# Kernel tuning notes

Hardware: AMD Instinct MI355X
Metric: run time of the kernel (lower is better)

Reference implementation:

```python
import jax, jax.numpy as jnp
import numpy as np

LN_EPS = 1e-5

def setup_inputs() -> dict:
    key = jax.random.key(0)
    ks = jax.random.split(key, 8)
    B, N, C = 8, 16384, 256
    x = jax.random.normal(ks[0], (B, N, C), dtype=jnp.float32)
    time_decay = jax.random.normal(ks[1], (C,), dtype=jnp.float32) * 0.1
    s = 1.0 / np.sqrt(C)
    W_k = jax.random.normal(ks[2], (C, C), dtype=jnp.float32) * s
    W_v = jax.random.normal(ks[3], (C, C), dtype=jnp.float32) * s
    W_r = jax.random.normal(ks[4], (C, C), dtype=jnp.float32) * s
    W_o = jax.random.normal(ks[5], (C, C), dtype=jnp.float32) * s
    ln_w = jnp.ones((C,), dtype=jnp.float32)
    ln_b = jnp.zeros((C,), dtype=jnp.float32)
    return {"x": x, "time_decay": time_decay, "W_k": W_k, "W_v": W_v,
            "W_r": W_r, "W_o": W_o, "ln_w": ln_w, "ln_b": ln_b}

def _layernorm(x, w, b):
    mu = jnp.mean(x, axis=-1, keepdims=True)
    var = jnp.mean(jnp.square(x - mu), axis=-1, keepdims=True)
    return (x - mu) * jax.lax.rsqrt(var + LN_EPS) * w + b

def reference(x, time_decay, W_k, W_v, W_r, W_o, ln_w, ln_b):
    # x: (B, N, C)
    xn = _layernorm(x, ln_w, ln_b)
    k = jnp.einsum('bnc,dc->bnd', xn, W_k)
    v = jnp.einsum('bnc,dc->bnd', xn, W_v)
    r = jax.nn.sigmoid(jnp.einsum('bnc,dc->bnd', xn, W_r))
    decay = jnp.exp(-jax.nn.relu(time_decay))  # (C,)

    def step(state, k_t):
        state = state * decay + k_t  # (B, C)
        return state, state

    k_tm = jnp.swapaxes(k, 0, 1)  # (N, B, C) time-major for scan
    init = jnp.zeros(k.shape[::2], dtype=x.dtype)  # (B, C)
    _, states = jax.lax.scan(step, init, k_tm)
    states = jnp.swapaxes(states, 0, 1)  # (B, N, C)
    y = r * (states + v)
    y = jnp.einsum('bnc,dc->bnd', y, W_o)
    return y
```

## Files before the change

### kernel.cpp

```cpp
#include <hip/hip_runtime.h>
#include <hip/hip_bf16.h>
#include <stdint.h>


typedef __attribute__((ext_vector_type(8))) short short8;
typedef __attribute__((ext_vector_type(4))) float f32x4;

static __device__ __forceinline__ unsigned short f2bf(float f) {
  __hip_bfloat16 h = __float2bfloat16(f);
  return *reinterpret_cast<unsigned short*>(&h);
}
static __device__ __forceinline__ float bf2f(unsigned short u) {
  unsigned int v = ((unsigned int)u) << 16;
  float f;
  __builtin_memcpy(&f, &v, 4);
  return f;
}

__global__ void ln_kernel(const float* __restrict__ x,
                          const float* __restrict__ w,
                          const float* __restrict__ b,
                          unsigned short* __restrict__ xn) {
  const int wv = threadIdx.x >> 6;
  const int ln = threadIdx.x & 63;
  const size_t row = (size_t)blockIdx.x * 4 + wv;
  const float4 v = reinterpret_cast<const float4*>(x)[row * 64 + ln];
  float s  = v.x + v.y + v.z + v.w;
  float sq = v.x * v.x + v.y * v.y + v.z * v.z + v.w * v.w;
#pragma unroll
  for (int off = 32; off; off >>= 1) {
    s  += __shfl_xor(s, off, 64);
    sq += __shfl_xor(sq, off, 64);
  }
  const float mu  = s * (1.0f / 256.0f);
  const float var = sq * (1.0f / 256.0f) - mu * mu;
  const float rs  = rsqrtf(var + 1e-5f);
  const float4 w4 = reinterpret_cast<const float4*>(w)[ln];
  const float4 b4 = reinterpret_cast<const float4*>(b)[ln];
  ushort4 o;
  o.x = f2bf((v.x - mu) * rs * w4.x + b4.x);
  o.y = f2bf((v.y - mu) * rs * w4.y + b4.y);
  o.z = f2bf((v.z - mu) * rs * w4.z + b4.z);
  o.w = f2bf((v.w - mu) * rs * w4.w + b4.w);
  reinterpret_cast<ushort4*>(xn)[row * 64 + ln] = o;
}

__global__ void cvt_weights(const float* __restrict__ Wk,
                            const float* __restrict__ Wv,
                            const float* __restrict__ Wr,
                            const float* __restrict__ Wo,
                            unsigned short* __restrict__ Wkvr,
                            unsigned short* __restrict__ Wob) {
  const int idx = blockIdx.x * 256 + threadIdx.x;
  if (idx < 768 * 256) {
    const int r = idx >> 8;
    const int c = idx & 255;
    const float* src = (r < 256) ? Wk : ((r < 512) ? Wv : Wr);
    Wkvr[idx] = f2bf(src[(r & 255) * 256 + c]);
  } else {
    const int j = idx - 768 * 256;
    Wob[j] = f2bf(Wo[j]);
  }
}

template <int EPI, int NY>
__global__ __launch_bounds__(512, 4) void gemm_bt(
    const unsigned short* __restrict__ A,
    const unsigned short* __restrict__ Bt,
    unsigned short* __restrict__ kbuf,
    unsigned short* __restrict__ vbuf,
    unsigned short* __restrict__ rbuf,
    float* __restrict__ outf) {
  constexpr int K = 256;
  __shared__ unsigned short Als[128][64];
  __shared__ unsigned short Bls[256][64];

  const int tid = threadIdx.x;
  const int wv = tid >> 6;
  const int ln = tid & 63;
  const int cpx = (int)gridDim.x >> 3;
  const int hw = (int)blockIdx.x;
  const int bid = (hw & 7) * cpx + (hw >> 3);
  const int bm0 = (bid / NY) * 128;
  const int bn0 = (bid % NY) * 256;
  const int lq = ln >> 4;
  const int lm = ln & 15;

  f32x4 acc[4][4];
#pragma unroll
  for (int i = 0; i < 4; ++i)
#pragma unroll
    for (int j = 0; j < 4; ++j) acc[i][j] = (f32x4){0.f, 0.f, 0.f, 0.f};

  const int m0w = (wv >> 2) * 64;
  const int n0w = (wv & 3) * 64;

  const int srow = ln >> 3;
  const int schunk = (ln & 7) ^ srow;

  const int ra = wv * 16;
  const int rb = wv * 32;

  for (int kk0 = 0; kk0 < K; kk0 += 64) {
    {
      const unsigned short* gA =
          A + (size_t)(bm0 + ra + srow) * K + kk0 + schunk * 8;
      __builtin_amdgcn_global_load_lds(
          (const __attribute__((address_space(1))) void*)gA,
          (__attribute__((address_space(3))) void*)&Als[ra][0], 16, 0, 0);
      __builtin_amdgcn_global_load_lds(
          (const __attribute__((address_space(1))) void*)(gA + 8 * K),
          (__attribute__((address_space(3))) void*)&Als[ra + 8][0], 16, 0, 0);
      const unsigned short* gB =
          Bt + (size_t)(bn0 + rb + srow) * K + kk0 + schunk * 8;
      __builtin_amdgcn_global_load_lds(
          (const __attribute__((address_space(1))) void*)gB,
          (__attribute__((address_space(3))) void*)&Bls[rb][0], 16, 0, 0);
      __builtin_amdgcn_global_load_lds(
          (const __attribute__((address_space(1))) void*)(gB + 8 * K),
          (__attribute__((address_space(3))) void*)&Bls[rb + 8][0], 16, 0, 0);
      __builtin_amdgcn_global_load_lds(
          (const __attribute__((address_space(1))) void*)(gB + 16 * K),
          (__attribute__((address_space(3))) void*)&Bls[rb + 16][0], 16, 0, 0);
      __builtin_amdgcn_global_load_lds(
          (const __attribute__((address_space(1))) void*)(gB + 24 * K),
          (__attribute__((address_space(3))) void*)&Bls[rb + 24][0], 16, 0, 0);
    }
    __syncthreads();
#pragma unroll
    for (int kk = 0; kk < 64; kk += 32) {
      short8 af[4], bfr[4];
      const int chunk = (kk >> 3) + lq;
      const int sw = chunk ^ (lm & 7);
#pragma unroll
      for (int t = 0; t < 4; ++t) {
        af[t] = *reinterpret_cast<const short8*>(&Als[m0w + t * 16 + lm][sw * 8]);
        bfr[t] = *reinterpret_cast<const short8*>(&Bls[n0w + t * 16 + lm][sw * 8]);
      }
#pragma unroll
      for (int mt = 0; mt < 4; ++mt)
#pragma unroll
        for (int nt = 0; nt < 4; ++nt)
          acc[mt][nt] = __builtin_amdgcn_mfma_f32_16x16x32_bf16(
              bfr[nt], af[mt], acc[mt][nt], 0, 0, 0);
    }
    __syncthreads();
  }

#pragma unroll
  for (int mt = 0; mt < 4; ++mt) {
    const int m_g = bm0 + m0w + mt * 16 + lm;
#pragma unroll
    for (int nt = 0; nt < 4; ++nt) {
      const int col = n0w + nt * 16 + lq * 4;
      f32x4 a = acc[mt][nt];
      if (EPI == 0) {
        const int bufi = bn0 >> 8;
        unsigned short* dst = (bufi == 0) ? kbuf : ((bufi == 1) ? vbuf : rbuf);
        if (bufi == 2) {
#pragma unroll
          for (int r = 0; r < 4; ++r) a[r] = 1.0f / (1.0f + __expf(-a[r]));
        }
        ushort4 pk;
        pk.x = f2bf(a[0]); pk.y = f2bf(a[1]); pk.z = f2bf(a[2]); pk.w = f2bf(a[3]);
        *reinterpret_cast<ushort4*>(&dst[(size_t)m_g * 256 + col]) = pk;
      } else {
        float4 o = make_float4(a[0], a[1], a[2], a[3]);
        *reinterpret_cast<float4*>(&outf[(size_t)m_g * 256 + col]) = o;
      }
    }
  }
}

__global__ void scan_carry(const unsigned short* __restrict__ k,
                           const float* __restrict__ td,
                           float* __restrict__ carry) {
  const int lane32 = threadIdx.x & 31;
  const int sub = threadIdx.x >> 5;
  const int bch = blockIdx.x * 8 + sub;
  const int c0 = lane32 * 8;
  float d[8], s[8];
#pragma unroll
  for (int j = 0; j < 8; ++j) {
    d[j] = expf(-fmaxf(td[c0 + j], 0.0f));
    s[j] = 0.0f;
  }
  const unsigned short* kp = k + (size_t)bch * 64 * 256 + c0;
#pragma unroll 4
  for (int i = 0; i < 64; ++i) {
    short8 kv = *reinterpret_cast<const short8*>(kp + (size_t)i * 256);
#pragma unroll
    for (int j = 0; j < 8; ++j) s[j] = s[j] * d[j] + bf2f((unsigned short)kv[j]);
  }
  float4* cp = reinterpret_cast<float4*>(carry + (size_t)bch * 256 + c0);
  cp[0] = make_float4(s[0], s[1], s[2], s[3]);
  cp[1] = make_float4(s[4], s[5], s[6], s[7]);
}

__global__ void scan_chunks(float* __restrict__ carry,
                            const float* __restrict__ td) {
  const int b = blockIdx.x;
  const int c = threadIdx.x;
  const float dL = expf(-fmaxf(td[c], 0.0f) * 64.0f);
  float s = 0.0f;
  float* base = carry + (size_t)b * 256 * 256 + c;
  for (int j0 = 0; j0 < 256; j0 += 8) {
    float buf[8];
#pragma unroll
    for (int t = 0; t < 8; ++t) buf[t] = base[(size_t)(j0 + t) * 256];
#pragma unroll
    for (int t = 0; t < 8; ++t) {
      base[(size_t)(j0 + t) * 256] = s;
      s = dL * s + buf[t];
    }
  }
}

__global__ void scan_final(unsigned short* __restrict__ k,
                           const unsigned short* __restrict__ v,
                           const unsigned short* __restrict__ r,
                           const float* __restrict__ carryin,
                           const float* __restrict__ td) {
  const int lane32 = threadIdx.x & 31;
  const int sub = threadIdx.x >> 5;
  const int bch = blockIdx.x * 8 + sub;
  const int c0 = lane32 * 8;
  float d[8], s[8];
  const float4* ci = reinterpret_cast<const float4*>(carryin + (size_t)bch * 256 + c0);
  float4 c0v = ci[0], c1v = ci[1];
  s[0] = c0v.x; s[1] = c0v.y; s[2] = c0v.z; s[3] = c0v.w;
  s[4] = c1v.x; s[5] = c1v.y; s[6] = c1v.z; s[7] = c1v.w;
#pragma unroll
  for (int j = 0; j < 8; ++j) d[j] = expf(-fmaxf(td[c0 + j], 0.0f));
  const size_t base = (size_t)bch * 64 * 256 + c0;
#pragma unroll 2
  for (int i = 0; i < 64; ++i) {
    const size_t off = base + (size_t)i * 256;
    short8 kv = *reinterpret_cast<const short8*>(k + off);
    short8 vv = *reinterpret_cast<const short8*>(v + off);
    short8 rv = *reinterpret_cast<const short8*>(r + off);
    short8 y;
#pragma unroll
    for (int j = 0; j < 8; ++j) {
      s[j] = s[j] * d[j] + bf2f((unsigned short)kv[j]);
      const float yj = bf2f((unsigned short)rv[j]) * (s[j] + bf2f((unsigned short)vv[j]));
      y[j] = (short)f2bf(yj);
    }
    *reinterpret_cast<short8*>(k + off) = y;
  }
}

extern "C" void kernel_launch(void* const* d_in, const int* in_sizes, int n_in,
                              void* d_out, int out_size, void* d_ws, size_t ws_size,
                              hipStream_t stream) {
  const float* x   = (const float*)d_in[0];
  const float* td  = (const float*)d_in[1];
  const float* Wk  = (const float*)d_in[2];
  const float* Wv  = (const float*)d_in[3];
  const float* Wr  = (const float*)d_in[4];
  const float* Wo  = (const float*)d_in[5];
  const float* lnw = (const float*)d_in[6];
  const float* lnb = (const float*)d_in[7];
  float* out = (float*)d_out;

  const int Bsz = 8, C = 256;
  const size_t M = 131072;

  char* ws = (char*)d_ws;
  size_t off = 0;
  auto alloc = [&](size_t bytes) -> char* {
    char* p = ws + off;
    off += (bytes + 255) & ~(size_t)255;
    return p;
  };
  unsigned short* xn   = (unsigned short*)alloc(M * C * 2);
  unsigned short* kbuf = (unsigned short*)alloc(M * C * 2);
  unsigned short* vbuf = (unsigned short*)alloc(M * C * 2);
  unsigned short* rbuf = (unsigned short*)alloc(M * C * 2);
  unsigned short* Wkvr = (unsigned short*)alloc(768 * 256 * 2);
  unsigned short* Wob  = (unsigned short*)alloc(256 * 256 * 2);
  float* carry = (float*)alloc((size_t)Bsz * 256 * C * 4);
  (void)ws_size; (void)in_sizes; (void)n_in; (void)out_size;

  cvt_weights<<<dim3(1024), dim3(256), 0, stream>>>(Wk, Wv, Wr, Wo, Wkvr, Wob);
  ln_kernel<<<dim3((unsigned)(M / 4)), dim3(256), 0, stream>>>(x, lnw, lnb, xn);
  gemm_bt<0, 3><<<dim3(3072), dim3(512), 0, stream>>>(
      xn, Wkvr, kbuf, vbuf, rbuf, nullptr);
  scan_carry<<<dim3(256), dim3(256), 0, stream>>>(kbuf, td, carry);
  scan_chunks<<<dim3(Bsz), dim3(256), 0, stream>>>(carry, td);
  scan_final<<<dim3(256), dim3(256), 0, stream>>>(kbuf, vbuf, rbuf, carry, td);
  gemm_bt<1, 1><<<dim3(1024), dim3(512), 0, stream>>>(
      kbuf, Wob, nullptr, nullptr, nullptr, out);
}
```

Measured before the change: 446.5 us.

## Load full-K A tile into LDS once, read B from global; widen scan parallelism

Measured after the change: 493.2 us. 1.1x slower.

```diff
diff --git a/kernel.cpp b/kernel.cpp
--- a/kernel.cpp
+++ b/kernel.cpp
@@ -4,6 +4,7 @@
 
 
 typedef __attribute__((ext_vector_type(8))) short short8;
+typedef __attribute__((ext_vector_type(4))) short short4v;
 typedef __attribute__((ext_vector_type(4))) float f32x4;
 
 static __device__ __forceinline__ unsigned short f2bf(float f) {
@@ -72,8 +73,7 @@
     unsigned short* __restrict__ rbuf,
     float* __restrict__ outf) {
   constexpr int K = 256;
-  __shared__ unsigned short Als[128][64];
-  __shared__ unsigned short Bls[256][64];
+  __shared__ unsigned short Als[128][256];
 
   const int tid = threadIdx.x;
   const int wv = tid >> 6;
@@ -95,56 +95,43 @@
   const int m0w = (wv >> 2) * 64;
   const int n0w = (wv & 3) * 64;
 
-  const int srow = ln >> 3;
-  const int schunk = (ln & 7) ^ srow;
-
-  const int ra = wv * 16;
-  const int rb = wv * 32;
-
-  for (int kk0 = 0; kk0 < K; kk0 += 64) {
-    {
+  {
+    const int rsub = ln >> 5;
+    const int p = ln & 31;
+#pragma unroll
+    for (int i = 0; i < 8; ++i) {
+      const int r0 = wv * 16 + i * 2;
+      const int r = r0 + rsub;
       const unsigned short* gA =
-          A + (size_t)(bm0 + ra + srow) * K + kk0 + schunk * 8;
+          A + (size_t)(bm0 + r) * K + ((p ^ (r & 7)) * 8);
       __builtin_amdgcn_global_load_lds(
           (const __attribute__((address_space(1))) void*)gA,
-          (__attribute__((address_space(3))) void*)&Als[ra][0], 16, 0, 0);
-      __builtin_amdgcn_global_load_lds(
-          (const __attribute__((address_space(1))) void*)(gA + 8 * K),
-          (__attribute__((address_space(3))) void*)&Als[ra + 8][0], 16, 0, 0);
-      const unsigned short* gB =
-          Bt + (size_t)(bn0 + rb + srow) * K + kk0 + schunk * 8;
-      __builtin_amdgcn_global_load_lds(
-          (const __attribute__((address_space(1))) void*)gB,
-          (__attribute__((address_space(3))) void*)&Bls[rb][0], 16, 0, 0);
-      __builtin_amdgcn_global_load_lds(
-          (const __attribute__((address_space(1))) void*)(gB + 8 * K),
-          (__attribute__((address_space(3))) void*)&Bls[rb + 8][0], 16, 0, 0);
-      __builtin_amdgcn_global_load_lds(
-          (const __attribute__((address_space(1))) void*)(gB + 16 * K),
-          (__attribute__((address_space(3))) void*)&Bls[rb + 16][0], 16, 0, 0);
-      __builtin_amdgcn_global_load_lds(
-          (const __attribute__((address_space(1))) void*)(gB + 24 * K),
-          (__attribute__((address_space(3))) void*)&Bls[rb + 24][0], 16, 0, 0);
-    }
-    __syncthreads();
-#pragma unroll
-    for (int kk = 0; kk < 64; kk += 32) {
-      short8 af[4], bfr[4];
-      const int chunk = (kk >> 3) + lq;
-      const int sw = chunk ^ (lm & 7);
-#pragma unroll
-      for (int t = 0; t < 4; ++t) {
-        af[t] = *reinterpret_cast<const short8*>(&Als[m0w + t * 16 + lm][sw * 8]);
-        bfr[t] = *reinterpret_cast<const short8*>(&Bls[n0w + t * 16 + lm][sw * 8]);
-      }
-#pragma unroll
-      for (int mt = 0; mt < 4; ++mt)
-#pragma unroll
-        for (int nt = 0; nt < 4; ++nt)
-          acc[mt][nt] = __builtin_amdgcn_mfma_f32_16x16x32_bf16(
-              bfr[nt], af[mt], acc[mt][nt], 0, 0, 0);
-    }
-    __syncthreads();
+          (__attribute__((address_space(3))) void*)&Als[r0][0], 16, 0, 0);
+    }
+  }
+  __syncthreads();
+
+  const unsigned short* Bbase =
+      Bt + (size_t)(bn0 + n0w + lm) * K + lq * 8;
+#pragma unroll 2
+  for (int ks = 0; ks < 8; ++ks) {
+    short8 bfr[4], af[4];
+#pragma unroll
+    for (int t = 0; t < 4; ++t)
+      bfr[t] = *reinterpret_cast<const short8*>(Bbase + (size_t)t * 16 * K +
+                                                ks * 32);
+#pragma unroll
+    for (int t = 0; t < 4; ++t) {
+      const int row = m0w + t * 16 + lm;
+      af[t] = *reinterpret_cast<const short8*>(
+          &Als[row][(((ks << 2) + lq) ^ (row & 7)) * 8]);
+    }
+#pragma unroll
+    for (int mt = 0; mt < 4; ++mt)
+#pragma unroll
+      for (int nt = 0; nt < 4; ++nt)
+        acc[mt][nt] = __builtin_amdgcn_mfma_f32_16x16x32_bf16(
+            bfr[nt], af[mt], acc[mt][nt], 0, 0, 0);
   }
 
 #pragma unroll
@@ -175,26 +162,25 @@
 __global__ void scan_carry(const unsigned short* __restrict__ k,
                            const float* __restrict__ td,
                            float* __restrict__ carry) {
-  const int lane32 = threadIdx.x & 31;
-  const int sub = threadIdx.x >> 5;
-  const int bch = blockIdx.x * 8 + sub;
-  const int c0 = lane32 * 8;
-  float d[8], s[8];
-#pragma unroll
-  for (int j = 0; j < 8; ++j) {
+  const int ln = threadIdx.x & 63;
+  const int w = threadIdx.x >> 6;
+  const int bch = blockIdx.x * 4 + w;
+  const int c0 = ln * 4;
+  float d[4], s[4];
+#pragma unroll
+  for (int j = 0; j < 4; ++j) {
     d[j] = expf(-fmaxf(td[c0 + j], 0.0f));
     s[j] = 0.0f;
   }
   const unsigned short* kp = k + (size_t)bch * 64 * 256 + c0;
-#pragma unroll 4
+#pragma unroll 8
   for (int i = 0; i < 64; ++i) {
-    short8 kv = *reinterpret_cast<const short8*>(kp + (size_t)i * 256);
-#pragma unroll
-    for (int j = 0; j < 8; ++j) s[j] = s[j] * d[j] + bf2f((unsigned short)kv[j]);
-  }
-  float4* cp = reinterpret_cast<float4*>(carry + (size_t)bch * 256 + c0);
-  cp[0] = make_float4(s[0], s[1], s[2], s[3]);
-  cp[1] = make_float4(s[4], s[5], s[6], s[7]);
+    short4v kv = *reinterpret_cast<const short4v*>(kp + (size_t)i * 256);
+#pragma unroll
+    for (int j = 0; j < 4; ++j) s[j] = s[j] * d[j] + bf2f((unsigned short)kv[j]);
+  }
+  *reinterpret_cast<float4*>(carry + (size_t)bch * 256 + c0) =
+      make_float4(s[0], s[1], s[2], s[3]);
 }
 
 __global__ void scan_chunks(float* __restrict__ carry,
@@ -221,32 +207,31 @@
                            const unsigned short* __restrict__ r,
                            const float* __restrict__ carryin,
                            const float* __restrict__ td) {
-  const int lane32 = threadIdx.x & 31;
-  const int sub = threadIdx.x >> 5;
-  const int bch = blockIdx.x * 8 + sub;
-  const int c0 = lane32 * 8;
-  float d[8], s[8];
-  const float4* ci = reinterpret_cast<const float4*>(carryin + (size_t)bch * 256 + c0);
-  float4 c0v = ci[0], c1v = ci[1];
-  s[0] = c0v.x; s[1] = c0v.y; s[2] = c0v.z; s[3] = c0v.w;
-  s[4] = c1v.x; s[5] = c1v.y; s[6] = c1v.z; s[7] = c1v.w;
-#pragma unroll
-  for (int j = 0; j < 8; ++j) d[j] = expf(-fmaxf(td[c0 + j], 0.0f));
+  const int ln = threadIdx.x & 63;
+  const int w = threadIdx.x >> 6;
+  const int bch = blockIdx.x * 4 + w;
+  const int c0 = ln * 4;
+  float d[4], s[4];
+  const float4 ci = *reinterpret_cast<const float4*>(
+      carryin + (size_t)bch * 256 + c0);
+  s[0] = ci.x; s[1] = ci.y; s[2] = ci.z; s[3] = ci.w;
+#pragma unroll
+  for (int j = 0; j < 4; ++j) d[j] = expf(-fmaxf(td[c0 + j], 0.0f));
   const size_t base = (size_t)bch * 64 * 256 + c0;
-#pragma unroll 2
+#pragma unroll 4
   for (int i = 0; i < 64; ++i) {
     const size_t off = base + (size_t)i * 256;
-    short8 kv = *reinterpret_cast<const short8*>(k + off);
-    short8 vv = *reinterpret_cast<const short8*>(v + off);
-    short8 rv = *reinterpret_cast<const short8*>(r + off);
-    short8 y;
-#pragma unroll
-    for (int j = 0; j < 8; ++j) {
+    short4v kv = *reinterpret_cast<const short4v*>(k + off);
+    short4v vv = *reinterpret_cast<const short4v*>(v + off);
+    short4v rv = *reinterpret_cast<const short4v*>(r + off);
+    short4v y;
+#pragma unroll
+    for (int j = 0; j < 4; ++j) {
       s[j] = s[j] * d[j] + bf2f((unsigned short)kv[j]);
       const float yj = bf2f((unsigned short)rv[j]) * (s[j] + bf2f((unsigned short)vv[j]));
       y[j] = (short)f2bf(yj);
     }
-    *reinterpret_cast<short8*>(k + off) = y;
+    *reinterpret_cast<short4v*>(k + off) = y;
   }
 }
 
@@ -286,9 +271,9 @@
   ln_kernel<<<dim3((unsigned)(M / 4)), dim3(256), 0, stream>>>(x, lnw, lnb, xn);
   gemm_bt<0, 3><<<dim3(3072), dim3(512), 0, stream>>>(
       xn, Wkvr, kbuf, vbuf, rbuf, nullptr);
-  scan_carry<<<dim3(256), dim3(256), 0, stream>>>(kbuf, td, carry);
+  scan_carry<<<dim3(512), dim3(256), 0, stream>>>(kbuf, td, carry);
   scan_chunks<<<dim3(Bsz), dim3(256), 0, stream>>>(carry, td);
-  scan_final<<<dim3(256), dim3(256), 0, stream>>>(kbuf, vbuf, rbuf, carry, td);
+  scan_final<<<dim3(512), dim3(256), 0, stream>>>(kbuf, vbuf, rbuf, carry, td);
   gemm_bt<1, 1><<<dim3(1024), dim3(512), 0, stream>>>(
       kbuf, Wob, nullptr, nullptr, nullptr, out);
 }
```
